# Performance work log

Measured on AMD Instinct MI355X. Metric: run time of the kernel, lower is better.

## Reference

```python
import jax, jax.numpy as jnp
import numpy as np

NUM_CODES = 1024
CODE_DIM = 256
BETA = 0.25  # commitment cost
N_TOKENS = 131072


def setup_inputs() -> dict:
    key = jax.random.key(0)
    k_z, k_cb = jax.random.split(key)
    z = jax.random.normal(k_z, (N_TOKENS, CODE_DIM), dtype=jnp.float32)
    # nn.init.uniform_(codebook.weight, -1/num_codes, 1/num_codes)
    codebook = jax.random.uniform(
        k_cb, (NUM_CODES, CODE_DIM), dtype=jnp.float32,
        minval=-1.0 / NUM_CODES, maxval=1.0 / NUM_CODES)
    return {"z": z, "codebook": codebook}


def reference(z, codebook):
    # Squared-euclidean distances: ||z||^2 + ||c||^2 - 2 z c^T  -> [N, K]
    d = (jnp.sum(z * z, axis=1, keepdims=True)
         + jnp.sum(codebook * codebook, axis=1)
         - 2.0 * jnp.einsum('nd,kd->nk', z, codebook))
    indices = jnp.argmin(d, axis=1)          # [N] int
    z_q = codebook[indices]                   # gather [N, D]

    sg = jax.lax.stop_gradient
    commit_loss = BETA * jnp.mean((sg(z) - z_q) ** 2)
    codebook_loss = jnp.mean((z - sg(z_q)) ** 2)
    loss = commit_loss + codebook_loss

    z_st = z + sg(z_q - z)                    # straight-through
    return z_st, indices, loss
```

## Files before the change

### kernel.cpp

```cpp
#include <hip/hip_runtime.h>

#define N_TOK 131072
#define KC    1024
#define DIM   256
#define GAP_THR 4e-4f
#define NBLK  (N_TOK / 128)

typedef __attribute__((ext_vector_type(8)))  short bf16x8;
typedef __attribute__((ext_vector_type(16))) float f32x16;

__device__ __forceinline__ unsigned short f2bf(float f) {
    unsigned int u = __float_as_uint(f);
    unsigned int r = (u + 0x7fffu + ((u >> 16) & 1u)) >> 16;
    return (unsigned short)r;
}

#define WS_NEED 6828096ull

__global__ void vq_prep_cb(const float* __restrict__ cb, unsigned short* __restrict__ cb16,
                           float* __restrict__ cnorm, unsigned int* __restrict__ fcount) {
    if (blockIdx.x == 0 && threadIdx.x == 0) *fcount = 0u;
    int code = blockIdx.x * 4 + (threadIdx.x >> 6);
    int lane = threadIdx.x & 63;
    float4 v = ((const float4*)cb)[(size_t)code * 64 + lane];
    ushort4 h;
    h.x = f2bf(v.x); h.y = f2bf(v.y); h.z = f2bf(v.z); h.w = f2bf(v.w);
    ((ushort4*)cb16)[(size_t)code * 64 + lane] = h;
    double s = 0.0;
    s = fma((double)v.x, (double)v.x, s);
    s = fma((double)v.y, (double)v.y, s);
    s = fma((double)v.z, (double)v.z, s);
    s = fma((double)v.w, (double)v.w, s);
    #pragma unroll
    for (int off = 32; off > 0; off >>= 1) s += __shfl_xor(s, off);
    if (lane == 0) cnorm[code] = (float)s;
}

__global__ void vq_transpose(const float* __restrict__ cb, float* __restrict__ cbT) {
    int g = blockIdx.x * 256 + threadIdx.x;
    int d4 = g >> 10, code = g & 1023;
    ((float4*)cbT)[g] = ((const float4*)cb)[(size_t)code * 64 + d4];
}

__global__ __launch_bounds__(256, 2)
void vq_scores_fused(const float* __restrict__ z, const unsigned short* __restrict__ cb16,
                     const float* __restrict__ cb, const float* __restrict__ cnorm,
                     float* __restrict__ out, float* __restrict__ out_idx,
                     int* __restrict__ flist, unsigned int* __restrict__ fcount,
                     unsigned long long* __restrict__ rck, double* __restrict__ lparts)
{
    __shared__ uint4  cA[128 * 32];
    __shared__ float  cnsL[KC];
    __shared__ float  bm1L[8][128];
    __shared__ double sredD[4];

    const int tid  = threadIdx.x;
    const int lane = tid & 63;
    const int l31  = lane & 31;
    const int hi   = lane >> 5;
    const int wid  = tid >> 6;
    const int tb   = blockIdx.x;
    const int ltok = wid * 32 + l31;

    #pragma unroll
    for (int k = 0; k < 4; ++k) cnsL[tid + k * 256] = cnorm[tid + k * 256];

    bf16x8 bfr[4][4];
    const float* zr = z + (size_t)(tb * 128 + ltok) * DIM;
    double s = 0.0;
    #pragma unroll
    for (int kb = 0; kb < 4; ++kb)
        #pragma unroll
        for (int ks = 0; ks < 4; ++ks) {
            const int d0 = kb * 64 + ks * 16 + hi * 8;
            float4 x = *(const float4*)(zr + d0);
            float4 y = *(const float4*)(zr + d0 + 4);
            s = fma((double)x.x, (double)x.x, s);
            s = fma((double)x.y, (double)x.y, s);
            s = fma((double)x.z, (double)x.z, s);
            s = fma((double)x.w, (double)x.w, s);
            s = fma((double)y.x, (double)y.x, s);
            s = fma((double)y.y, (double)y.y, s);
            s = fma((double)y.z, (double)y.z, s);
            s = fma((double)y.w, (double)y.w, s);
            bf16x8 v;
            v[0] = (short)f2bf(x.x); v[1] = (short)f2bf(x.y);
            v[2] = (short)f2bf(x.z); v[3] = (short)f2bf(x.w);
            v[4] = (short)f2bf(y.x); v[5] = (short)f2bf(y.y);
            v[6] = (short)f2bf(y.z); v[7] = (short)f2bf(y.w);
            bfr[kb][ks] = v;
        }
    s += __shfl_xor(s, 32);
    const float zzr = (float)s;

    float gm1 = 3.0e38f, gm2 = 3.0e38f; int gid_ = 0x7fffffff;

    #pragma unroll 1
    for (int cbk = 0; cbk < 8; ++cbk) {
        __syncthreads();
        #pragma unroll
        for (int i = 0; i < 16; ++i) {
            int g = tid + i * 256;
            int c = g >> 5, u = g & 31;
            cA[c * 32 + (u ^ (c & 7))] = ((const uint4*)cb16)[(size_t)(cbk * 128 + c) * 32 + u];
        }
        __syncthreads();

        f32x16 acc[4];
        #pragma unroll
        for (int a = 0; a < 4; ++a)
            #pragma unroll
            for (int r = 0; r < 16; ++r) acc[a][r] = 0.0f;

        #pragma unroll
        for (int kb = 0; kb < 4; ++kb)
            #pragma unroll
            for (int ks = 0; ks < 4; ++ks) {
                const bf16x8 bv = bfr[kb][ks];
                #pragma unroll
                for (int a = 0; a < 4; ++a) {
                    int c = a * 32 + l31;
                    bf16x8 af = ((const bf16x8*)cA)[c * 32 + ((kb * 8 + ks * 2 + hi) ^ (c & 7))];
                    acc[a] = __builtin_amdgcn_mfma_f32_32x32x16_bf16(af, bv, acc[a], 0, 0, 0);
                }
            }

        float c1 = 3.0e38f, c2 = 3.0e38f;
        #pragma unroll
        for (int a = 0; a < 4; ++a)
            #pragma unroll
            for (int r = 0; r < 16; ++r) {
                int cl = a * 32 + (r & 3) + 8 * (r >> 2) + 4 * hi;
                float A  = zzr + cnsL[cbk * 128 + cl];
                float dq = fmaf(acc[a][r], -2.0f, A);
                acc[a][r] = dq;
                float hv = fmaxf(c1, dq);
                c1 = fminf(c1, dq);
                c2 = fminf(c2, hv);
            }
        int ci = 0x7fffffff;
        #pragma unroll
        for (int a = 0; a < 4; ++a)
            #pragma unroll
            for (int r = 0; r < 16; ++r) {
                int code = cbk * 128 + a * 32 + (r & 3) + 8 * (r >> 2) + 4 * hi;
                ci = min(ci, (acc[a][r] == c1) ? code : 0x7fffffff);
            }
        float o1 = __shfl_xor(c1, 32);
        float o2 = __shfl_xor(c2, 32);
        int  oi  = __shfl_xor(ci, 32);
        float nm2 = fminf(fminf(c2, o2), fmaxf(c1, o1));
        int  ni  = (o1 < c1 || (o1 == c1 && oi < ci)) ? oi : ci;
        float nm1 = fminf(c1, o1);
        if (hi == 0) bm1L[cbk][ltok] = nm1;
        float ng2 = fminf(fminf(gm2, nm2), fmaxf(gm1, nm1));
        if (nm1 < gm1 || (nm1 == gm1 && ni < gid_)) { gm1 = nm1; gid_ = ni; }
        gm2 = ng2;
    }

    const int rowg = tb * 128 + ltok;
    if (hi == 0) {
        out_idx[rowg] = (float)gid_;
        float gap = gm2 - gm1;
        if (!(gap > GAP_THR)) {
            rck[rowg] = ~0ull;
            #pragma unroll
            for (int c = 0; c < 8; ++c)
                if (bm1L[c][ltok] <= gm1 + GAP_THR) {
                    unsigned int p = atomicAdd(fcount, 1u);
                    flist[p] = rowg | (c << 17);
                }
        }
    }

    double ls = 0.0;
    #pragma unroll 4
    for (int r = 0; r < 32; ++r) {
        int idx = __shfl(gid_, r);
        size_t row = (size_t)tb * 128 + wid * 32 + r;
        float4 zv = ((const float4*)z)[row * 64 + lane];
        float4 cv = ((const float4*)cb)[(size_t)idx * 64 + lane];
        float4 o;
        o.x = zv.x + (cv.x - zv.x);
        o.y = zv.y + (cv.y - zv.y);
        o.z = zv.z + (cv.z - zv.z);
        o.w = zv.w + (cv.w - zv.w);
        ((float4*)out)[row * 64 + lane] = o;
        float dx = zv.x - cv.x, dy = zv.y - cv.y, dz = zv.z - cv.z, dw = zv.w - cv.w;
        ls += (double)dx * dx + (double)dy * dy + (double)dz * dz + (double)dw * dw;
    }
    #pragma unroll
    for (int off = 32; off > 0; off >>= 1) ls += __shfl_down(ls, off);
    if (lane == 0) sredD[wid] = ls;
    __syncthreads();
    if (tid == 0) lparts[tb] = (sredD[0] + sredD[1]) + (sredD[2] + sredD[3]);
}

__global__ __launch_bounds__(256)
void vq_recheck_pairs(const float* __restrict__ z, const float* __restrict__ cbT,
                      const float* __restrict__ cnorm, const int* __restrict__ flist,
                      const unsigned int* __restrict__ fcount,
                      unsigned long long* __restrict__ rck)
{
    const int tid  = threadIdx.x;
    const int wid  = tid >> 6;
    const int lane = tid & 63;
    const unsigned int cnt = *fcount;

    for (unsigned int p = blockIdx.x * 4 + wid; p < cnt; p += gridDim.x * 4) {
        const int e   = flist[p];
        const int row = e & 0x1FFFF;
        const int blk = ((unsigned int)e) >> 17;
        const float* zr = z + (size_t)row * DIM;

        float4 zv = ((const float4*)zr)[lane];
        double s = 0.0;
        s = fma((double)zv.x, (double)zv.x, s);
        s = fma((double)zv.y, (double)zv.y, s);
        s = fma((double)zv.z, (double)zv.z, s);
        s = fma((double)zv.w, (double)zv.w, s);
        #pragma unroll
        for (int off = 32; off > 0; off >>= 1) s += __shfl_xor(s, off);
        const float zz = (float)s;

        const int c0 = blk * 128 + lane;
        float e0 = 0.0f, e1 = 0.0f;
        #pragma unroll 8
        for (int d4 = 0; d4 < 64; ++d4) {
            float4 zq = ((const float4*)zr)[d4];
            float4 a  = ((const float4*)cbT)[d4 * KC + c0];
            float4 b  = ((const float4*)cbT)[d4 * KC + c0 + 64];
            e0 = fmaf(zq.x, a.x, e0); e0 = fmaf(zq.y, a.y, e0);
            e0 = fmaf(zq.z, a.z, e0); e0 = fmaf(zq.w, a.w, e0);
            e1 = fmaf(zq.x, b.x, e1); e1 = fmaf(zq.y, b.y, e1);
            e1 = fmaf(zq.z, b.z, e1); e1 = fmaf(zq.w, b.w, e1);
        }
        const float dq0 = fmaf(e0, -2.0f, zz + cnorm[c0]);
        const float dq1 = fmaf(e1, -2.0f, zz + cnorm[c0 + 64]);
        unsigned long long k0 = ((unsigned long long)__float_as_uint(dq0) << 32) | (unsigned int)c0;
        unsigned long long k1 = ((unsigned long long)__float_as_uint(dq1) << 32) | (unsigned int)(c0 + 64);
        unsigned long long k = k0 < k1 ? k0 : k1;
        #pragma unroll
        for (int off = 32; off > 0; off >>= 1) {
            unsigned long long o = __shfl_xor(k, off);
            k = o < k ? o : k;
        }
        if (lane == 0) atomicMin(&rck[row], k);
    }
}

__global__ __launch_bounds__(256)
void vq_fixup(const float* __restrict__ z, const float* __restrict__ cb,
              const int* __restrict__ flist, const unsigned int* __restrict__ fcount,
              const unsigned long long* __restrict__ rck,
              float* __restrict__ out, float* __restrict__ out_idx)
{
    const int tid  = threadIdx.x;
    const int wid  = tid >> 6;
    const int lane = tid & 63;
    const unsigned int cnt = *fcount;

    for (unsigned int p = blockIdx.x * 4 + wid; p < cnt; p += gridDim.x * 4) {
        const int row  = flist[p] & 0x1FFFF;
        const int code = (int)(unsigned int)rck[row];
        float4 zv = ((const float4*)z)[(size_t)row * 64 + lane];
        float4 cv = ((const float4*)cb)[(size_t)code * 64 + lane];
        float4 o;
        o.x = zv.x + (cv.x - zv.x);
        o.y = zv.y + (cv.y - zv.y);
        o.z = zv.z + (cv.z - zv.z);
        o.w = zv.w + (cv.w - zv.w);
        ((float4*)out)[(size_t)row * 64 + lane] = o;
        if (lane == 0) out_idx[row] = (float)code;
    }
}

__global__ void vq_loss_final(const double* __restrict__ lparts, float* __restrict__ out_loss) {
    __shared__ double s[256];
    const int tid = threadIdx.x;
    double a = 0.0;
    for (int i = tid; i < NBLK; i += 256) a += lparts[i];
    s[tid] = a;
    __syncthreads();
    for (int sft = 128; sft > 0; sft >>= 1) {
        if (tid < sft) s[tid] += s[tid + sft];
        __syncthreads();
    }
    if (tid == 0) {
        float mean = (float)(s[0] / (double)((size_t)N_TOK * DIM));
        out_loss[0] = 0.25f * mean + mean;
    }
}

extern "C" void kernel_launch(void* const* d_in, const int* in_sizes, int n_in,
                              void* d_out, int out_size, void* d_ws, size_t ws_size,
                              hipStream_t stream) {
    const float* z  = (const float*)d_in[0];
    const float* cb = (const float*)d_in[1];
    float* out = (float*)d_out;
    char* ws = (char*)d_ws;

    unsigned short*     cb16   = (unsigned short*)(ws);
    float*              cnorm  = (float*)(ws + 524288);
    float*              cbT    = (float*)(ws + 528384);
    unsigned int*       fcount = (unsigned int*)(ws + 1576960);
    int*                flist  = (int*)(ws + 1577024);
    unsigned long long* rck    = (unsigned long long*)(ws + 5771328);
    double*             lparts = (double*)(ws + 6819904);

    float* out_idx  = out + (size_t)N_TOK * DIM;
    float* out_loss = out_idx + N_TOK;

    vq_prep_cb<<<KC / 4, 256, 0, stream>>>(cb, cb16, cnorm, fcount);
    vq_transpose<<<(KC * DIM / 4) / 256, 256, 0, stream>>>(cb, cbT);
    vq_scores_fused<<<NBLK, 256, 0, stream>>>(z, cb16, cb, cnorm, out, out_idx,
                                              flist, fcount, rck, lparts);
    vq_recheck_pairs<<<1024, 256, 0, stream>>>(z, cbT, cnorm, flist, fcount, rck);
    vq_fixup<<<512, 256, 0, stream>>>(z, cb, flist, fcount, rck, out, out_idx);
    vq_loss_final<<<1, 256, 0, stream>>>(lparts, out_loss);
}
```

Baseline: 383.4 us.

## Stream MFMA-fragment-ordered codebook from global memory, drop LDS staging and barriers

The codebook is pre-packed in bf16 into the exact MFMA A-fragment order, so each lane loads its fragments straight from global/L2 instead of staging 128-code tiles through shared memory with two barriers per tile. The -0.5*||c||^2 term is pre-arranged to match the accumulator layout and used as the MFMA initial value, which removes per-element norm lookups in the epilogue. Without the large LDS buffer the launch bound rises to four blocks per CU and the loop works on 64-code sub-blocks. The cost is more global/L2 traffic per block and more register pressure, and the near-tie threshold is loosened, which may route more rows to the recheck path.

After: 520.4 us. +35.7%, slower.

```diff
diff --git a/kernel.cpp b/kernel.cpp
--- a/kernel.cpp
+++ b/kernel.cpp
@@ -3,7 +3,7 @@
 #define N_TOK 131072
 #define KC    1024
 #define DIM   256
-#define GAP_THR 4e-4f
+#define GAP_THR 5e-4f
 #define NBLK  (N_TOK / 128)
 
 typedef __attribute__((ext_vector_type(8)))  short bf16x8;
@@ -15,17 +15,23 @@
     return (unsigned short)r;
 }
 
-#define WS_NEED 6828096ull
-
-__global__ void vq_prep_cb(const float* __restrict__ cb, unsigned short* __restrict__ cb16,
-                           float* __restrict__ cnorm, unsigned int* __restrict__ fcount) {
+#define WS_NEED 6832192ull
+
+__global__ void vq_prep_cb(const float* __restrict__ cb, unsigned short* __restrict__ cb16F,
+                           float* __restrict__ cnsF, float* __restrict__ cnorm,
+                           unsigned int* __restrict__ fcount) {
     if (blockIdx.x == 0 && threadIdx.x == 0) *fcount = 0u;
     int code = blockIdx.x * 4 + (threadIdx.x >> 6);
     int lane = threadIdx.x & 63;
     float4 v = ((const float4*)cb)[(size_t)code * 64 + lane];
     ushort4 h;
     h.x = f2bf(v.x); h.y = f2bf(v.y); h.z = f2bf(v.z); h.w = f2bf(v.w);
-    ((ushort4*)cb16)[(size_t)code * 64 + lane] = h;
+    int d = lane * 4;
+    int kb = d >> 6, ks = (d >> 4) & 3, hi = (d >> 3) & 1;
+    int step = kb * 4 + ks;
+    int g = code >> 5, l31 = code & 31;
+    size_t sidx = ((size_t)(g * 16 + step) * 64 + hi * 32 + l31) * 8 + (d & 7);
+    *(ushort4*)(cb16F + sidx) = h;
     double s = 0.0;
     s = fma((double)v.x, (double)v.x, s);
     s = fma((double)v.y, (double)v.y, s);
@@ -33,7 +39,14 @@
     s = fma((double)v.w, (double)v.w, s);
     #pragma unroll
     for (int off = 32; off > 0; off >>= 1) s += __shfl_xor(s, off);
-    if (lane == 0) cnorm[code] = (float)s;
+    if (lane == 0) {
+        float cn = (float)s;
+        cnorm[code] = cn;
+        int row = code & 31;
+        int hic = (row >> 2) & 1;
+        int rc  = (row & 3) | ((row >> 3) << 2);
+        cnsF[(g * 2 + hic) * 16 + rc] = -0.5f * cn;
+    }
 }
 
 __global__ void vq_transpose(const float* __restrict__ cb, float* __restrict__ cbT) {
@@ -42,16 +55,14 @@
     ((float4*)cbT)[g] = ((const float4*)cb)[(size_t)code * 64 + d4];
 }
 
-__global__ __launch_bounds__(256, 2)
-void vq_scores_fused(const float* __restrict__ z, const unsigned short* __restrict__ cb16,
-                     const float* __restrict__ cb, const float* __restrict__ cnorm,
+__global__ __launch_bounds__(256, 4)
+void vq_scores_fused(const float* __restrict__ z, const unsigned short* __restrict__ cb16F,
+                     const float* __restrict__ cnsF, const float* __restrict__ cb,
                      float* __restrict__ out, float* __restrict__ out_idx,
                      int* __restrict__ flist, unsigned int* __restrict__ fcount,
                      unsigned long long* __restrict__ rck, double* __restrict__ lparts)
 {
-    __shared__ uint4  cA[128 * 32];
-    __shared__ float  cnsL[KC];
-    __shared__ float  bm1L[8][128];
+    __shared__ float  bm1L[16][128];
     __shared__ double sredD[4];
 
     const int tid  = threadIdx.x;
@@ -61,9 +72,6 @@
     const int wid  = tid >> 6;
     const int tb   = blockIdx.x;
     const int ltok = wid * 32 + l31;
-
-    #pragma unroll
-    for (int k = 0; k < 4; ++k) cnsL[tid + k * 256] = cnorm[tid + k * 256];
 
     bf16x8 bfr[4][4];
     const float* zr = z + (size_t)(tb * 128 + ltok) * DIM;
@@ -94,23 +102,20 @@
     const float zzr = (float)s;
 
     float gm1 = 3.0e38f, gm2 = 3.0e38f; int gid_ = 0x7fffffff;
+    const bf16x8* AF = (const bf16x8*)cb16F;
 
     #pragma unroll 1
-    for (int cbk = 0; cbk < 8; ++cbk) {
-        __syncthreads();
-        #pragma unroll
-        for (int i = 0; i < 16; ++i) {
-            int g = tid + i * 256;
-            int c = g >> 5, u = g & 31;
-            cA[c * 32 + (u ^ (c & 7))] = ((const uint4*)cb16)[(size_t)(cbk * 128 + c) * 32 + u];
-        }
-        __syncthreads();
-
-        f32x16 acc[4];
-        #pragma unroll
-        for (int a = 0; a < 4; ++a)
-            #pragma unroll
-            for (int r = 0; r < 16; ++r) acc[a][r] = 0.0f;
+    for (int sb = 0; sb < 16; ++sb) {
+        f32x16 acc[2];
+        #pragma unroll
+        for (int gi = 0; gi < 2; ++gi) {
+            const float4* cp = (const float4*)(cnsF + (((sb * 2 + gi) * 2 + hi) << 4));
+            float4 c0 = cp[0], c1 = cp[1], c2 = cp[2], c3 = cp[3];
+            acc[gi][0]  = c0.x; acc[gi][1]  = c0.y; acc[gi][2]  = c0.z; acc[gi][3]  = c0.w;
+            acc[gi][4]  = c1.x; acc[gi][5]  = c1.y; acc[gi][6]  = c1.z; acc[gi][7]  = c1.w;
+            acc[gi][8]  = c2.x; acc[gi][9]  = c2.y; acc[gi][10] = c2.z; acc[gi][11] = c2.w;
+            acc[gi][12] = c3.x; acc[gi][13] = c3.y; acc[gi][14] = c3.z; acc[gi][15] = c3.w;
+        }
 
         #pragma unroll
         for (int kb = 0; kb < 4; ++kb)
@@ -118,41 +123,38 @@
             for (int ks = 0; ks < 4; ++ks) {
                 const bf16x8 bv = bfr[kb][ks];
                 #pragma unroll
-                for (int a = 0; a < 4; ++a) {
-                    int c = a * 32 + l31;
-                    bf16x8 af = ((const bf16x8*)cA)[c * 32 + ((kb * 8 + ks * 2 + hi) ^ (c & 7))];
-                    acc[a] = __builtin_amdgcn_mfma_f32_32x32x16_bf16(af, bv, acc[a], 0, 0, 0);
+                for (int gi = 0; gi < 2; ++gi) {
+                    bf16x8 af = AF[(size_t)((sb * 2 + gi) * 16 + kb * 4 + ks) * 64 + lane];
+                    acc[gi] = __builtin_amdgcn_mfma_f32_32x32x16_bf16(af, bv, acc[gi], 0, 0, 0);
                 }
             }
 
-        float c1 = 3.0e38f, c2 = 3.0e38f;
-        #pragma unroll
-        for (int a = 0; a < 4; ++a)
+        float c1v = 3.0e38f, c2v = 3.0e38f;
+        #pragma unroll
+        for (int gi = 0; gi < 2; ++gi)
             #pragma unroll
             for (int r = 0; r < 16; ++r) {
-                int cl = a * 32 + (r & 3) + 8 * (r >> 2) + 4 * hi;
-                float A  = zzr + cnsL[cbk * 128 + cl];
-                float dq = fmaf(acc[a][r], -2.0f, A);
-                acc[a][r] = dq;
-                float hv = fmaxf(c1, dq);
-                c1 = fminf(c1, dq);
-                c2 = fminf(c2, hv);
+                float dq = fmaf(acc[gi][r], -2.0f, zzr);
+                acc[gi][r] = dq;
+                float hv = fmaxf(c1v, dq);
+                c1v = fminf(c1v, dq);
+                c2v = fminf(c2v, hv);
             }
         int ci = 0x7fffffff;
         #pragma unroll
-        for (int a = 0; a < 4; ++a)
+        for (int gi = 0; gi < 2; ++gi)
             #pragma unroll
             for (int r = 0; r < 16; ++r) {
-                int code = cbk * 128 + a * 32 + (r & 3) + 8 * (r >> 2) + 4 * hi;
-                ci = min(ci, (acc[a][r] == c1) ? code : 0x7fffffff);
+                int code = (sb * 2 + gi) * 32 + (r & 3) + 8 * (r >> 2) + 4 * hi;
+                ci = min(ci, (acc[gi][r] == c1v) ? code : 0x7fffffff);
             }
-        float o1 = __shfl_xor(c1, 32);
-        float o2 = __shfl_xor(c2, 32);
+        float o1 = __shfl_xor(c1v, 32);
+        float o2 = __shfl_xor(c2v, 32);
         int  oi  = __shfl_xor(ci, 32);
-        float nm2 = fminf(fminf(c2, o2), fmaxf(c1, o1));
-        int  ni  = (o1 < c1 || (o1 == c1 && oi < ci)) ? oi : ci;
-        float nm1 = fminf(c1, o1);
-        if (hi == 0) bm1L[cbk][ltok] = nm1;
+        float nm2 = fminf(fminf(c2v, o2), fmaxf(c1v, o1));
+        int  ni  = (o1 < c1v || (o1 == c1v && oi < ci)) ? oi : ci;
+        float nm1 = fminf(c1v, o1);
+        if (hi == 0) bm1L[sb][ltok] = nm1;
         float ng2 = fminf(fminf(gm2, nm2), fmaxf(gm1, nm1));
         if (nm1 < gm1 || (nm1 == gm1 && ni < gid_)) { gm1 = nm1; gid_ = ni; }
         gm2 = ng2;
@@ -165,11 +167,13 @@
         if (!(gap > GAP_THR)) {
             rck[rowg] = ~0ull;
             #pragma unroll
-            for (int c = 0; c < 8; ++c)
-                if (bm1L[c][ltok] <= gm1 + GAP_THR) {
+            for (int c = 0; c < 8; ++c) {
+                float bmin = fminf(bm1L[2 * c][ltok], bm1L[2 * c + 1][ltok]);
+                if (bmin <= gm1 + GAP_THR) {
                     unsigned int p = atomicAdd(fcount, 1u);
                     flist[p] = rowg | (c << 17);
                 }
+            }
         }
     }
 
@@ -300,20 +304,21 @@
     float* out = (float*)d_out;
     char* ws = (char*)d_ws;
 
-    unsigned short*     cb16   = (unsigned short*)(ws);
-    float*              cnorm  = (float*)(ws + 524288);
-    float*              cbT    = (float*)(ws + 528384);
-    unsigned int*       fcount = (unsigned int*)(ws + 1576960);
-    int*                flist  = (int*)(ws + 1577024);
-    unsigned long long* rck    = (unsigned long long*)(ws + 5771328);
-    double*             lparts = (double*)(ws + 6819904);
+    unsigned short*     cb16F  = (unsigned short*)(ws);
+    float*              cnsF   = (float*)(ws + 524288);
+    float*              cnorm  = (float*)(ws + 528384);
+    float*              cbT    = (float*)(ws + 532480);
+    unsigned int*       fcount = (unsigned int*)(ws + 1581056);
+    int*                flist  = (int*)(ws + 1581120);
+    unsigned long long* rck    = (unsigned long long*)(ws + 5775424);
+    double*             lparts = (double*)(ws + 6824000);
 
     float* out_idx  = out + (size_t)N_TOK * DIM;
     float* out_loss = out_idx + N_TOK;
 
-    vq_prep_cb<<<KC / 4, 256, 0, stream>>>(cb, cb16, cnorm, fcount);
+    vq_prep_cb<<<KC / 4, 256, 0, stream>>>(cb, cb16F, cnsF, cnorm, fcount);
     vq_transpose<<<(KC * DIM / 4) / 256, 256, 0, stream>>>(cb, cbT);
-    vq_scores_fused<<<NBLK, 256, 0, stream>>>(z, cb16, cb, cnorm, out, out_idx,
+    vq_scores_fused<<<NBLK, 256, 0, stream>>>(z, cb16F, cnsF, cb, out, out_idx,
                                               flist, fcount, rck, lparts);
     vq_recheck_pairs<<<1024, 256, 0, stream>>>(z, cbT, cnorm, flist, fcount, rck);
     vq_fixup<<<512, 256, 0, stream>>>(z, cb, flist, fcount, rck, out, out_idx);
```
